# Optimization experiments

Measured on AMD Instinct MI355X. Metric: run time of the kernel, lower is better.

The kernel has to match this reference:

```python
import jax, jax.numpy as jnp
from jax import lax
import numpy as np

K = 3          # kernel_size (must be 3 for shape consistency with the 3x3 sigma conv)
STRIDE = 2
C_IN = 128
EPS = 1e-5     # FrozenBatchNorm2d eps


def setup_inputs() -> dict:
    key = jax.random.key(0)
    k1, k2, k3, k4, k5, k6 = jax.random.split(key, 6)
    x = jax.random.normal(k1, (8, C_IN, 112, 112), dtype=jnp.float32)
    # conv: in_channels -> k*k, 3x3, no bias (kaiming init ~ normal scaled)
    fan_out = K * K * 3 * 3
    conv_w = jax.random.normal(k2, (K * K, C_IN, 3, 3), dtype=jnp.float32) * np.sqrt(2.0 / fan_out)
    bn_w = jax.random.normal(k3, (K * K,), dtype=jnp.float32) * 0.1 + 1.0
    bn_b = jax.random.normal(k4, (K * K,), dtype=jnp.float32) * 0.1
    bn_mean = jax.random.normal(k5, (K * K,), dtype=jnp.float32) * 0.1
    bn_var = jax.random.uniform(k6, (K * K,), dtype=jnp.float32, minval=0.5, maxval=1.5)
    return {"x": x, "conv_w": conv_w, "bn_w": bn_w, "bn_b": bn_b,
            "bn_mean": bn_mean, "bn_var": bn_var}


def _pasa(x, conv_w, bn_w, bn_b, bn_mean, bn_var):
    n, c, h, w = x.shape
    pad = K // 2
    # reflection pad
    xp = jnp.pad(x, ((0, 0), (0, 0), (pad, pad), (pad, pad)), mode="reflect")
    # 3x3 conv, stride 1, VALID on padded input -> same h, w
    sigma = lax.conv_general_dilated(xp, conv_w, (1, 1), "VALID",
                                     dimension_numbers=("NCHW", "OIHW", "NCHW"))
    # frozen BN: affine with fixed running stats
    scale = bn_w / jnp.sqrt(bn_var + EPS)
    shift = bn_b - bn_mean * scale
    sigma = sigma * scale[None, :, None, None] + shift[None, :, None, None]
    sigma = jnp.clip(sigma, 0.0001)                       # clamp min only
    sigma = sigma.reshape(n, 1, K * K, h * w)
    sigma = sigma / jnp.sum(sigma, axis=2, keepdims=True)  # normalize over k*k
    # unfold: k*k shifted views of the padded input (channel-outer, kernel row-major)
    patches = jnp.stack([xp[:, :, i:i + h, j:j + w]
                         for i in range(K) for j in range(K)], axis=2)  # (n,c,9,h,w)
    out = jnp.sum(patches.reshape(n, c, K * K, h * w) * sigma, axis=2).reshape(n, c, h, w)
    return out[:, :, ::STRIDE, ::STRIDE]


def reference(x, conv_w, bn_w, bn_b, bn_mean, bn_var):
    return _pasa(x, conv_w, bn_w, bn_b, bn_mean, bn_var)
```

## Files before the change

### kernel.cpp

```cpp
#include <hip/hip_runtime.h>
#include <hip/hip_bf16.h>

#define NB   8
#define C    128
#define H    112
#define W    112
#define HW   (H * W)
#define HO   56
#define WO   56
#define KK   9
#define WAVES 16
#define CPW  8
#define NPAIR (C / 2)
#define PPW  (CPW / 2)
#define WPK_ELEMS (NPAIR * 81)
#define SHIFT_OFF (WPK_ELEMS * 2)

__global__ void pasa_prep(const float* __restrict__ cw,
                          const float* __restrict__ bw,
                          const float* __restrict__ bb,
                          const float* __restrict__ bm,
                          const float* __restrict__ bv,
                          float* __restrict__ ws) {
    int idx = blockIdx.x * 256 + threadIdx.x;
    if (idx < WPK_ELEMS) {
        int cip = idx / 81;
        int rem = idx % 81;
        int kh = rem / 27;
        int r2 = rem % 27;
        int k  = r2 / 3;
        int kw = r2 % 3;
        float scale = bw[k] / sqrtf(bv[k] + 1e-5f);
        int ca = 2 * cip, cb = 2 * cip + 1;
        ws[2 * idx + 0] = cw[((k * C + ca) * 3 + kh) * 3 + kw] * scale;
        ws[2 * idx + 1] = cw[((k * C + cb) * 3 + kh) * 3 + kw] * scale;
    } else if (idx < WPK_ELEMS + KK) {
        int k = idx - WPK_ELEMS;
        float scale = bw[k] / sqrtf(bv[k] + 1e-5f);
        ws[SHIFT_OFF + k] = bb[k] - bm[k] * scale;
    }
}

__device__ inline float2 pkfma(float2 a, float2 b, float2 c) {
    float2 r;
    r.x = fmaf(a.x, b.x, c.x);
    r.y = fmaf(a.y, b.y, c.y);
    return r;
}

__global__ __launch_bounds__(1024, 4)
void pasa_main(const float* __restrict__ x,
               const float2* __restrict__ wpk,
               const float* __restrict__ shift,
               float* __restrict__ out) {
    __shared__ float part[WAVES * KK * 64];
    __shared__ float sig[KK * 57];

    const int bid  = blockIdx.x;
    const int n    = bid & 7;
    const int ho   = bid >> 3;
    const int tid  = threadIdx.x;
    const int lane = tid & 63;
    const int wv   = __builtin_amdgcn_readfirstlane(tid >> 6);
    const int wo   = lane < WO ? lane : (WO - 1);

    int rows[3];
    rows[0] = (ho == 0) ? 1 : (2 * ho - 1);
    rows[1] = 2 * ho;
    rows[2] = 2 * ho + 1;

    const float* xn = x + (size_t)n * C * HW;
    const int p0 = wv * PPW;

    float2 va[PPW][3], vb[PPW][3];
#pragma unroll
    for (int p = 0; p < PPW; ++p) {
        const float* xa = xn + (size_t)(2 * (p0 + p)) * HW;
        const float* xb = xa + HW;
#pragma unroll
        for (int kh = 0; kh < 3; ++kh) {
            va[p][kh] = *(const float2*)(xa + rows[kh] * W + 2 * wo);
            vb[p][kh] = *(const float2*)(xb + rows[kh] * W + 2 * wo);
        }
    }

    float2 acc[KK];
#pragma unroll
    for (int k = 0; k < KK; ++k) acc[k] = make_float2(0.0f, 0.0f);

#pragma unroll
    for (int p = 0; p < PPW; ++p) {
        const float2* wb = wpk + (p0 + p) * 81;
#pragma unroll
        for (int kh = 0; kh < 3; ++kh) {
            float2 t1 = make_float2(va[p][kh].x, vb[p][kh].x);
            float2 t2 = make_float2(va[p][kh].y, vb[p][kh].y);
            float2 t0;
            t0.x = __shfl_up(t2.x, 1);
            t0.y = __shfl_up(t2.y, 1);
            const float2* wr = wb + kh * 27;
#pragma unroll
            for (int k = 0; k < KK; ++k)
                acc[k] = pkfma(t2, wr[3 * k + 2],
                          pkfma(t1, wr[3 * k + 1],
                          pkfma(t0, wr[3 * k + 0], acc[k])));
        }
    }

#pragma unroll
    for (int k = 0; k < KK; ++k)
        part[(wv * KK + k) * 64 + lane] = acc[k].x + acc[k].y;
    __syncthreads();

    if (tid < KK * WO) {
        const int k = tid / WO;
        const int w_ = tid % WO;
        float s = 0.0f;
#pragma unroll
        for (int w2 = 0; w2 < WAVES; ++w2) s += part[(w2 * KK + k) * 64 + w_];
        s += shift[k];
        s = fmaxf(s, 1e-4f);
        sig[k * 57 + w_] = s;
    }
    __syncthreads();

    float sg[KK];
    float tot = 0.0f;
#pragma unroll
    for (int k = 0; k < KK; ++k) { sg[k] = sig[k * 57 + wo]; tot += sg[k]; }
    const float inv = 1.0f / tot;
#pragma unroll
    for (int k = 0; k < KK; ++k) sg[k] *= inv;

    float* on = out + ((size_t)n * C) * (HO * WO) + ho * WO;
#pragma unroll
    for (int p = 0; p < PPW; ++p) {
        float oa = 0.0f, ob = 0.0f;
#pragma unroll
        for (int kh = 0; kh < 3; ++kh) {
            const float a1 = va[p][kh].x, a2 = va[p][kh].y;
            const float b1 = vb[p][kh].x, b2 = vb[p][kh].y;
            const float a0 = __shfl_up(a2, 1);
            const float b0 = __shfl_up(b2, 1);
            oa = fmaf(a0, sg[kh * 3 + 0],
                 fmaf(a1, sg[kh * 3 + 1],
                 fmaf(a2, sg[kh * 3 + 2], oa)));
            ob = fmaf(b0, sg[kh * 3 + 0],
                 fmaf(b1, sg[kh * 3 + 1],
                 fmaf(b2, sg[kh * 3 + 2], ob)));
        }
        if (lane < WO) {
            const int ci = 2 * (p0 + p);
            on[(size_t)ci * (HO * WO) + lane]       = oa;
            on[(size_t)(ci + 1) * (HO * WO) + lane] = ob;
        }
    }
}

extern "C" void kernel_launch(void* const* d_in, const int* in_sizes, int n_in,
                              void* d_out, int out_size, void* d_ws, size_t ws_size,
                              hipStream_t stream) {
    const float* x   = (const float*)d_in[0];
    const float* cw  = (const float*)d_in[1];
    const float* bw  = (const float*)d_in[2];
    const float* bb  = (const float*)d_in[3];
    const float* bm  = (const float*)d_in[4];
    const float* bv  = (const float*)d_in[5];
    float* ws  = (float*)d_ws;
    float* out = (float*)d_out;

    const int prep_elems = WPK_ELEMS + KK;
    pasa_prep<<<(prep_elems + 255) / 256, 256, 0, stream>>>(cw, bw, bb, bm, bv, ws);
    pasa_main<<<NB * HO, 1024, 0, stream>>>(x, (const float2*)ws,
                                            ws + SHIFT_OFF, out);
}
```

Before: 110.2 us.

## Process two output rows per block with row reuse and prefetch

Each block now computes two consecutive output rows, reusing the shared input row between them and loading the next two rows while the first row's reduction runs. The grid is halved. Packed-FMA intrinsics via ext_vector_type and nontemporal output stores are also added. This cuts redundant input loads and overlaps memory latency with compute, at the cost of higher register pressure and fewer blocks.

Measured after the change: 110.3 us. Within noise of the previous version (+0.1%).

```diff
diff --git a/kernel.cpp b/kernel.cpp
--- a/kernel.cpp
+++ b/kernel.cpp
@@ -1,5 +1,4 @@
 #include <hip/hip_runtime.h>
-#include <hip/hip_bf16.h>
 
 #define NB   8
 #define C    128
@@ -15,6 +14,8 @@
 #define PPW  (CPW / 2)
 #define WPK_ELEMS (NPAIR * 81)
 #define SHIFT_OFF (WPK_ELEMS * 2)
+
+typedef float v2f __attribute__((ext_vector_type(2)));
 
 __global__ void pasa_prep(const float* __restrict__ cw,
                           const float* __restrict__ bw,
@@ -41,16 +42,13 @@
     }
 }
 
-__device__ inline float2 pkfma(float2 a, float2 b, float2 c) {
-    float2 r;
-    r.x = fmaf(a.x, b.x, c.x);
-    r.y = fmaf(a.y, b.y, c.y);
-    return r;
+__device__ inline v2f pkfma(v2f a, v2f b, v2f c) {
+    return __builtin_elementwise_fma(a, b, c);
 }
 
 __global__ __launch_bounds__(1024, 4)
 void pasa_main(const float* __restrict__ x,
-               const float2* __restrict__ wpk,
+               const v2f* __restrict__ wpk,
                const float* __restrict__ shift,
                float* __restrict__ out) {
     __shared__ float part[WAVES * KK * 64];
@@ -58,101 +56,129 @@
 
     const int bid  = blockIdx.x;
     const int n    = bid & 7;
-    const int ho   = bid >> 3;
+    const int hb   = bid >> 3;
     const int tid  = threadIdx.x;
     const int lane = tid & 63;
     const int wv   = __builtin_amdgcn_readfirstlane(tid >> 6);
     const int wo   = lane < WO ? lane : (WO - 1);
 
-    int rows[3];
-    rows[0] = (ho == 0) ? 1 : (2 * ho - 1);
-    rows[1] = 2 * ho;
-    rows[2] = 2 * ho + 1;
+    const int r0 = (hb == 0) ? 1 : (4 * hb - 1);
+    const int r1 = 4 * hb;
+    const int r2 = 4 * hb + 1;
+    const int r3 = 4 * hb + 2;
+    const int r4 = 4 * hb + 3;
 
     const float* xn = x + (size_t)n * C * HW;
     const int p0 = wv * PPW;
 
-    float2 va[PPW][3], vb[PPW][3];
+    v2f va[PPW][3], vb[PPW][3];
 #pragma unroll
     for (int p = 0; p < PPW; ++p) {
-        const float* xa = xn + (size_t)(2 * (p0 + p)) * HW;
+        const float* xa = xn + (size_t)(2 * (p0 + p)) * HW + 2 * wo;
         const float* xb = xa + HW;
-#pragma unroll
-        for (int kh = 0; kh < 3; ++kh) {
-            va[p][kh] = *(const float2*)(xa + rows[kh] * W + 2 * wo);
-            vb[p][kh] = *(const float2*)(xb + rows[kh] * W + 2 * wo);
-        }
+        va[p][0] = *(const v2f*)(xa + r0 * W);
+        va[p][1] = *(const v2f*)(xa + r1 * W);
+        va[p][2] = *(const v2f*)(xa + r2 * W);
+        vb[p][0] = *(const v2f*)(xb + r0 * W);
+        vb[p][1] = *(const v2f*)(xb + r1 * W);
+        vb[p][2] = *(const v2f*)(xb + r2 * W);
     }
 
-    float2 acc[KK];
-#pragma unroll
-    for (int k = 0; k < KK; ++k) acc[k] = make_float2(0.0f, 0.0f);
-
-#pragma unroll
-    for (int p = 0; p < PPW; ++p) {
-        const float2* wb = wpk + (p0 + p) * 81;
-#pragma unroll
-        for (int kh = 0; kh < 3; ++kh) {
-            float2 t1 = make_float2(va[p][kh].x, vb[p][kh].x);
-            float2 t2 = make_float2(va[p][kh].y, vb[p][kh].y);
-            float2 t0;
-            t0.x = __shfl_up(t2.x, 1);
-            t0.y = __shfl_up(t2.y, 1);
-            const float2* wr = wb + kh * 27;
-#pragma unroll
-            for (int k = 0; k < KK; ++k)
-                acc[k] = pkfma(t2, wr[3 * k + 2],
-                          pkfma(t1, wr[3 * k + 1],
-                          pkfma(t0, wr[3 * k + 0], acc[k])));
-        }
-    }
-
-#pragma unroll
-    for (int k = 0; k < KK; ++k)
-        part[(wv * KK + k) * 64 + lane] = acc[k].x + acc[k].y;
-    __syncthreads();
-
-    if (tid < KK * WO) {
-        const int k = tid / WO;
-        const int w_ = tid % WO;
-        float s = 0.0f;
-#pragma unroll
-        for (int w2 = 0; w2 < WAVES; ++w2) s += part[(w2 * KK + k) * 64 + w_];
-        s += shift[k];
-        s = fmaxf(s, 1e-4f);
-        sig[k * 57 + w_] = s;
-    }
-    __syncthreads();
-
-    float sg[KK];
-    float tot = 0.0f;
-#pragma unroll
-    for (int k = 0; k < KK; ++k) { sg[k] = sig[k * 57 + wo]; tot += sg[k]; }
-    const float inv = 1.0f / tot;
-#pragma unroll
-    for (int k = 0; k < KK; ++k) sg[k] *= inv;
-
-    float* on = out + ((size_t)n * C) * (HO * WO) + ho * WO;
-#pragma unroll
-    for (int p = 0; p < PPW; ++p) {
-        float oa = 0.0f, ob = 0.0f;
-#pragma unroll
-        for (int kh = 0; kh < 3; ++kh) {
-            const float a1 = va[p][kh].x, a2 = va[p][kh].y;
-            const float b1 = vb[p][kh].x, b2 = vb[p][kh].y;
-            const float a0 = __shfl_up(a2, 1);
-            const float b0 = __shfl_up(b2, 1);
-            oa = fmaf(a0, sg[kh * 3 + 0],
-                 fmaf(a1, sg[kh * 3 + 1],
-                 fmaf(a2, sg[kh * 3 + 2], oa)));
-            ob = fmaf(b0, sg[kh * 3 + 0],
-                 fmaf(b1, sg[kh * 3 + 1],
-                 fmaf(b2, sg[kh * 3 + 2], ob)));
-        }
-        if (lane < WO) {
-            const int ci = 2 * (p0 + p);
-            on[(size_t)ci * (HO * WO) + lane]       = oa;
-            on[(size_t)(ci + 1) * (HO * WO) + lane] = ob;
+    v2f ta[PPW][2], tb[PPW][2];
+    float* on_base = out + (size_t)n * C * (HO * WO);
+
+#pragma unroll
+    for (int half = 0; half < 2; ++half) {
+        v2f acc[KK];
+#pragma unroll
+        for (int k = 0; k < KK; ++k) acc[k] = (v2f){0.0f, 0.0f};
+
+#pragma unroll
+        for (int p = 0; p < PPW; ++p) {
+            const v2f* wb = wpk + (p0 + p) * 81;
+#pragma unroll
+            for (int kh = 0; kh < 3; ++kh) {
+                v2f t1 = { va[p][kh].x, vb[p][kh].x };
+                v2f t2 = { va[p][kh].y, vb[p][kh].y };
+                v2f t0;
+                t0.x = __shfl_up(t2.x, 1);
+                t0.y = __shfl_up(t2.y, 1);
+                const v2f* wr = wb + kh * 27;
+#pragma unroll
+                for (int k = 0; k < KK; ++k)
+                    acc[k] = pkfma(t2, wr[3 * k + 2],
+                              pkfma(t1, wr[3 * k + 1],
+                              pkfma(t0, wr[3 * k + 0], acc[k])));
+            }
+        }
+
+#pragma unroll
+        for (int k = 0; k < KK; ++k)
+            part[(wv * KK + k) * 64 + lane] = acc[k].x + acc[k].y;
+
+        if (half == 0) {
+#pragma unroll
+            for (int p = 0; p < PPW; ++p) {
+                const float* xa = xn + (size_t)(2 * (p0 + p)) * HW + 2 * wo;
+                const float* xb = xa + HW;
+                ta[p][0] = *(const v2f*)(xa + r3 * W);
+                ta[p][1] = *(const v2f*)(xa + r4 * W);
+                tb[p][0] = *(const v2f*)(xb + r3 * W);
+                tb[p][1] = *(const v2f*)(xb + r4 * W);
+            }
+        }
+        __syncthreads();
+
+        if (tid < KK * WO) {
+            const int k = tid / WO;
+            const int w_ = tid % WO;
+            float s = 0.0f;
+#pragma unroll
+            for (int w2 = 0; w2 < WAVES; ++w2) s += part[(w2 * KK + k) * 64 + w_];
+            s += shift[k];
+            s = fmaxf(s, 1e-4f);
+            sig[k * 57 + w_] = s;
+        }
+        __syncthreads();
+
+        float sg[KK];
+        float tot = 0.0f;
+#pragma unroll
+        for (int k = 0; k < KK; ++k) { sg[k] = sig[k * 57 + wo]; tot += sg[k]; }
+        const float inv = 1.0f / tot;
+#pragma unroll
+        for (int k = 0; k < KK; ++k) sg[k] *= inv;
+
+        const int ho = 2 * hb + half;
+        float* on = on_base + (size_t)ho * WO;
+#pragma unroll
+        for (int p = 0; p < PPW; ++p) {
+            v2f o = (v2f){0.0f, 0.0f};
+#pragma unroll
+            for (int kh = 0; kh < 3; ++kh) {
+                v2f t1 = { va[p][kh].x, vb[p][kh].x };
+                v2f t2 = { va[p][kh].y, vb[p][kh].y };
+                v2f t0;
+                t0.x = __shfl_up(t2.x, 1);
+                t0.y = __shfl_up(t2.y, 1);
+                v2f s0 = { sg[kh * 3 + 0], sg[kh * 3 + 0] };
+                v2f s1 = { sg[kh * 3 + 1], sg[kh * 3 + 1] };
+                v2f s2 = { sg[kh * 3 + 2], sg[kh * 3 + 2] };
+                o = pkfma(t2, s2, pkfma(t1, s1, pkfma(t0, s0, o)));
+            }
+            if (lane < WO) {
+                const int ci = 2 * (p0 + p);
+                __builtin_nontemporal_store(o.x, on + (size_t)ci * (HO * WO) + lane);
+                __builtin_nontemporal_store(o.y, on + (size_t)(ci + 1) * (HO * WO) + lane);
+            }
+        }
+
+        if (half == 0) {
+#pragma unroll
+            for (int p = 0; p < PPW; ++p) {
+                va[p][0] = va[p][2]; va[p][1] = ta[p][0]; va[p][2] = ta[p][1];
+                vb[p][0] = vb[p][2]; vb[p][1] = tb[p][0]; vb[p][2] = tb[p][1];
+            }
         }
     }
 }
@@ -171,6 +197,6 @@
 
     const int prep_elems = WPK_ELEMS + KK;
     pasa_prep<<<(prep_elems + 255) / 256, 256, 0, stream>>>(cw, bw, bb, bm, bv, ws);
-    pasa_main<<<NB * HO, 1024, 0, stream>>>(x, (const float2*)ws,
-                                            ws + SHIFT_OFF, out);
-}
+    pasa_main<<<NB * (HO / 2), 1024, 0, stream>>>(x, (const v2f*)ws,
+                                                  ws + SHIFT_OFF, out);
+}
```
